# Kernel optimization log

Hardware: AMD Instinct MI355X
Metric: run time of the kernel (lower is better)

Reference implementation:

```python
import jax, jax.numpy as jnp
import numpy as np

B, S, D, H = 4, 2048, 1024, 16
DH = D // H  # attention_head_size = 64


def setup_inputs() -> dict:
    key = jax.random.key(0)
    ks = jax.random.split(key, 9)
    scale = 1.0 / np.sqrt(D)
    x = jax.random.normal(ks[0], (B, S, D), dtype=jnp.float32)
    Wq = jax.random.normal(ks[1], (H, D, DH), dtype=jnp.float32) * scale
    Wk = jax.random.normal(ks[2], (H, D, DH), dtype=jnp.float32) * scale
    Wv = jax.random.normal(ks[3], (H, D, DH), dtype=jnp.float32) * scale
    bq = jax.random.normal(ks[4], (H, DH), dtype=jnp.float32) * 0.01
    bk = jax.random.normal(ks[5], (H, DH), dtype=jnp.float32) * 0.01
    bv = jax.random.normal(ks[6], (H, DH), dtype=jnp.float32) * 0.01
    Wo = jax.random.normal(ks[7], (D, D), dtype=jnp.float32) * scale
    bo = jax.random.normal(ks[8], (D,), dtype=jnp.float32) * 0.01
    return {"x": x, "Wq": Wq, "bq": bq, "Wk": Wk, "bk": bk,
            "Wv": Wv, "bv": bv, "Wo": Wo, "bo": bo}


def reference(x, Wq, bq, Wk, bk, Wv, bv, Wo, bo):
    # Per-head Linear projections, stacked over the head axis h.
    q = jnp.einsum('bsd,hde->bhse', x, Wq) + bq[None, :, None, :]
    k = jnp.einsum('bsd,hde->bhse', x, Wk) + bk[None, :, None, :]
    v = jnp.einsum('bsd,hde->bhse', x, Wv) + bv[None, :, None, :]
    # QK^T / sqrt(dh), softmax over keys (axis=-1), then @ V.
    scores = jnp.einsum('bhse,bhte->bhst', q, k) / jnp.sqrt(jnp.float32(DH))
    attn = jax.nn.softmax(scores, axis=-1)
    ctx = jnp.einsum('bhst,bhte->bhse', attn, v)
    # Concatenate heads along the feature axis: [B,S,H*DH].
    concat = jnp.transpose(ctx, (0, 2, 1, 3)).reshape(B, S, H * DH)
    # Output projection (dropout is identity in inference).
    return concat @ Wo + bo
```

## Files before the change

### kernel.cpp

```cpp
#include <hip/hip_runtime.h>


#define Bn  4
#define Sn  2048
#define Dn  1024
#define Hn  16
#define DHn 64
#define Mn  (Bn*Sn)
#define LDKV 72

typedef unsigned short u16;
typedef __attribute__((ext_vector_type(8))) short short8;
typedef __attribute__((ext_vector_type(4))) short short4v;
typedef __attribute__((ext_vector_type(4))) float f32x4;
typedef __attribute__((ext_vector_type(2))) unsigned int uint2v;

__device__ __forceinline__ u16 f2bf(float f) {
  unsigned u = __float_as_uint(f);
  return (u16)((u + 0x7FFFu + ((u >> 16) & 1u)) >> 16);
}

__device__ __forceinline__ void async16(const void* g, void* l) {
  __builtin_amdgcn_global_load_lds(
      (const __attribute__((address_space(1))) void*)g,
      (__attribute__((address_space(3))) void*)l, 16, 0, 0);
}

__device__ __forceinline__ unsigned pk2(float a, float b) {
  return __builtin_amdgcn_perm(__float_as_uint(b), __float_as_uint(a), 0x07060302u);
}

__global__ __launch_bounds__(256) void k_convert_x(
    const float4* __restrict__ x, ushort4* __restrict__ xb, int n4) {
  int i = blockIdx.x * 256 + threadIdx.x;
  if (i < n4) {
    float4 f = x[i];
    ushort4 o;
    o.x = f2bf(f.x); o.y = f2bf(f.y); o.z = f2bf(f.z); o.w = f2bf(f.w);
    xb[i] = o;
  }
}

__global__ __launch_bounds__(256) void k_convert_w(
    const float* __restrict__ Wq, const float* __restrict__ Wk,
    const float* __restrict__ Wv, const float* __restrict__ Wo,
    u16* __restrict__ WqT, u16* __restrict__ WkT,
    u16* __restrict__ WvT, u16* __restrict__ WoT) {
  __shared__ float t[64][65];
  const int bid = blockIdx.x;
  const int wsel = bid >> 8;
  const int idx = bid & 255;
  const int tid = threadIdx.x;
  const int c = tid & 63;
  const int r4 = tid >> 6;

  if (wsel < 3) {
    const float* W = (wsel == 0) ? Wq : (wsel == 1) ? Wk : Wv;
    u16* T = (wsel == 0) ? WqT : (wsel == 1) ? WkT : WvT;
    const int h = idx >> 4;
    const int d0 = (idx & 15) * 64;
    const float* src = W + (size_t)h * (Dn * DHn) + (size_t)d0 * DHn;
#pragma unroll
    for (int r = 0; r < 16; r++) {
      int row = r * 4 + r4;
      t[row][c] = src[row * DHn + c];
    }
    __syncthreads();
    u16* dst = T + (size_t)(h * 64) * Dn + d0;
#pragma unroll
    for (int r = 0; r < 16; r++) {
      int erow = r * 4 + r4;
      dst[(size_t)erow * Dn + c] = f2bf(t[c][erow]);
    }
  } else {
    const int n0 = (idx >> 4) * 64;
    const int d0 = (idx & 15) * 64;
#pragma unroll
    for (int r = 0; r < 16; r++) {
      int row = r * 4 + r4;
      t[row][c] = Wo[(size_t)(d0 + row) * Dn + n0 + c];
    }
    __syncthreads();
#pragma unroll
    for (int r = 0; r < 16; r++) {
      int nrow = r * 4 + r4;
      WoT[(size_t)(n0 + nrow) * Dn + d0 + c] = f2bf(t[c][nrow]);
    }
  }
}

template<int SWAP>
__global__ __launch_bounds__(512) void k_gemm_qkv(
    const u16* __restrict__ A, const u16* __restrict__ B0T,
    const u16* __restrict__ B1T, const float* __restrict__ bias0,
    const float* __restrict__ bias1, u16* __restrict__ out0,
    u16* __restrict__ out1) {
  const int z = blockIdx.z;
  const u16* BT = z ? B1T : B0T;
  const float* bias = z ? bias1 : bias0;
  u16* dst = z ? out1 : out0;
  const int tile_m = blockIdx.x * 128;
  const int tile_n = blockIdx.y * 128;
  const int K = Dn;

  __shared__ u16 As[128 * 64];
  __shared__ u16 Bs[128 * 64];

  const int tid = threadIdx.x;
  const int lane = tid & 63;
  const int wave = tid >> 6;
  const int wm = wave & 3, wn = wave >> 2;
  const int quad = lane >> 4, l16 = lane & 15;
  const int srow8 = lane >> 3;
  const int gchunk = (lane & 7) ^ srow8;
  const int sw = l16 & 7;

  f32x4 acc[2][4];
#pragma unroll
  for (int i = 0; i < 2; i++)
#pragma unroll
    for (int j = 0; j < 4; j++) acc[i][j] = (f32x4){0.f, 0.f, 0.f, 0.f};

  for (int k0 = 0; k0 < K; k0 += 64) {
    const int rb = wave * 16;
    async16(&A[(size_t)(tile_m + rb + srow8) * K + k0 + gchunk * 8], &As[rb * 64]);
    async16(&A[(size_t)(tile_m + rb + 8 + srow8) * K + k0 + gchunk * 8], &As[(rb + 8) * 64]);
    async16(&BT[(size_t)(tile_n + rb + srow8) * K + k0 + gchunk * 8], &Bs[rb * 64]);
    async16(&BT[(size_t)(tile_n + rb + 8 + srow8) * K + k0 + gchunk * 8], &Bs[(rb + 8) * 64]);
    __syncthreads();
#pragma unroll
    for (int ks = 0; ks < 2; ++ks) {
      short8 a[2], b[4];
#pragma unroll
      for (int i = 0; i < 2; i++)
        a[i] = *(const short8*)&As[(wm * 32 + i * 16 + l16) * 64 + ((ks * 4 + quad) ^ sw) * 8];
#pragma unroll
      for (int j = 0; j < 4; j++)
        b[j] = *(const short8*)&Bs[(wn * 64 + j * 16 + l16) * 64 + ((ks * 4 + quad) ^ sw) * 8];
#pragma unroll
      for (int i = 0; i < 2; i++)
#pragma unroll
        for (int j = 0; j < 4; j++)
          acc[i][j] = SWAP
              ? __builtin_amdgcn_mfma_f32_16x16x32_bf16(b[j], a[i], acc[i][j], 0, 0, 0)
              : __builtin_amdgcn_mfma_f32_16x16x32_bf16(a[i], b[j], acc[i][j], 0, 0, 0);
    }
    __syncthreads();
  }

  if (SWAP) {
    const float scale = (z == 0) ? 0.18033688011112042f : 1.0f;
#pragma unroll
    for (int i = 0; i < 2; i++) {
      const int s = tile_m + wm * 32 + i * 16 + l16;
      const int bb = s >> 11, sl = s & 2047;
#pragma unroll
      for (int j = 0; j < 4; j++) {
        const int nb = tile_n + wn * 64 + j * 16 + quad * 4;
        const float4 b4 = *(const float4*)&bias[nb];
        const int h = nb >> 6, e0 = nb & 63;
        ushort4 o;
        o.x = f2bf((acc[i][j][0] + b4.x) * scale);
        o.y = f2bf((acc[i][j][1] + b4.y) * scale);
        o.z = f2bf((acc[i][j][2] + b4.z) * scale);
        o.w = f2bf((acc[i][j][3] + b4.w) * scale);
        *(ushort4*)&dst[((size_t)(bb * Hn + h) * Sn + sl) * DHn + e0] = o;
      }
    }
  } else {
#pragma unroll
    for (int i = 0; i < 2; i++) {
      const int s0 = tile_m + wm * 32 + i * 16 + quad * 4;
      const int bb = s0 >> 11, sl = s0 & 2047;
#pragma unroll
      for (int j = 0; j < 4; j++) {
        const int n = tile_n + wn * 64 + j * 16 + l16;
        const int h = n >> 6, e = n & 63;
        const float bn = bias[n];
        ushort4 o;
        o.x = f2bf(acc[i][j][0] + bn);
        o.y = f2bf(acc[i][j][1] + bn);
        o.z = f2bf(acc[i][j][2] + bn);
        o.w = f2bf(acc[i][j][3] + bn);
        *(ushort4*)&dst[((size_t)(bb * Hn + h) * DHn + e) * Sn + sl] = o;
      }
    }
  }
}

__global__ __launch_bounds__(256) void k_attn(
    const u16* __restrict__ qg, const u16* __restrict__ kg,
    const u16* __restrict__ vg, u16* __restrict__ ctx) {
  const int bh = blockIdx.y;
  const int b = bh >> 4, h = bh & 15;
  const int tid = threadIdx.x;
  const int wave = tid >> 6, lane = tid & 63;
  const int quad = lane >> 4, l16 = lane & 15;
  const int qbase = blockIdx.x * 128 + wave * 32;

  const u16* qp = qg + (size_t)bh * Sn * DHn;
  const u16* kp = kg + (size_t)bh * Sn * DHn;
  const u16* vp = vg + (size_t)bh * DHn * Sn;

  __shared__ u16 Ks[2][64 * 64];
  __shared__ u16 Vs[2][64 * LDKV];

  const int srow8 = lane >> 3;
  const int gchunk = (lane & 7) ^ srow8;
  const int sw = l16 & 7;

  const int vrow = tid >> 3;
  const int vc = tid & 7;

  short8 bq[2][2];
#pragma unroll
  for (int g2 = 0; g2 < 2; g2++) {
    bq[g2][0] = *(const short8*)&qp[(size_t)(qbase + g2 * 16 + l16) * DHn + quad * 8];
    bq[g2][1] = *(const short8*)&qp[(size_t)(qbase + g2 * 16 + l16) * DHn + 32 + quad * 8];
  }

  f32x4 octx[2][4];
#pragma unroll
  for (int g2 = 0; g2 < 2; g2++)
#pragma unroll
    for (int j = 0; j < 4; j++) octx[g2][j] = (f32x4){0.f, 0.f, 0.f, 0.f};
  float lr[2] = {0.f, 0.f};

  {
    const int rbase = wave * 16;
    async16(&kp[(size_t)(rbase + srow8) * DHn + gchunk * 8], &Ks[0][rbase * 64]);
    async16(&kp[(size_t)(rbase + 8 + srow8) * DHn + gchunk * 8], &Ks[0][(rbase + 8) * 64]);
    uint4 vv0 = *(const uint4*)&vp[(size_t)vrow * Sn + vc * 8];
    uint4 vv1 = *(const uint4*)&vp[(size_t)(32 + vrow) * Sn + vc * 8];
    *(uint4*)&Vs[0][vrow * LDKV + vc * 8] = vv0;
    *(uint4*)&Vs[0][(32 + vrow) * LDKV + vc * 8] = vv1;
  }
  __syncthreads();

  uint4 vv0, vv1;
  for (int kt = 0; kt < Sn / 64; ++kt) {
    const int cur = kt & 1, nxt = cur ^ 1;
    const bool more = (kt + 1 < Sn / 64);
    if (more) {
      const int key1 = (kt + 1) * 64;
      const int rbase = wave * 16;
      async16(&kp[(size_t)(key1 + rbase + srow8) * DHn + gchunk * 8], &Ks[nxt][rbase * 64]);
      async16(&kp[(size_t)(key1 + rbase + 8 + srow8) * DHn + gchunk * 8], &Ks[nxt][(rbase + 8) * 64]);
      vv0 = *(const uint4*)&vp[(size_t)vrow * Sn + key1 + vc * 8];
      vv1 = *(const uint4*)&vp[(size_t)(32 + vrow) * Sn + key1 + vc * 8];
    }

    short4v ap[2][4];
#pragma unroll
    for (int g = 0; g < 4; g++) {
      short8 ka0 = *(const short8*)&Ks[cur][(g * 16 + l16) * 64 + (quad ^ sw) * 8];
      short8 ka1 = *(const short8*)&Ks[cur][(g * 16 + l16) * 64 + ((quad + 4) ^ sw) * 8];
#pragma unroll
      for (int g2 = 0; g2 < 2; g2++) {
        f32x4 sc = (f32x4){0.f, 0.f, 0.f, 0.f};
        sc = __builtin_amdgcn_mfma_f32_16x16x32_bf16(ka0, bq[g2][0], sc, 0, 0, 0);
        sc = __builtin_amdgcn_mfma_f32_16x16x32_bf16(ka1, bq[g2][1], sc, 0, 0, 0);
        float p[4];
#pragma unroll
        for (int r = 0; r < 4; r++) p[r] = __builtin_amdgcn_exp2f(sc[r]);
        lr[g2] += (p[0] + p[1]) + (p[2] + p[3]);
        ap[g2][g] = __builtin_bit_cast(short4v,
            (uint2v){pk2(p[0], p[1]), pk2(p[2], p[3])});
      }
    }

#pragma unroll
    for (int j = 0; j < 4; j++) {
#pragma unroll
      for (int g = 0; g < 4; g++) {
        short4v vb = *(const short4v*)&Vs[cur][(j * 16 + l16) * LDKV + g * 16 + quad * 4];
        octx[0][j] = __builtin_amdgcn_mfma_f32_16x16x16bf16_1k(ap[0][g], vb, octx[0][j], 0, 0, 0);
        octx[1][j] = __builtin_amdgcn_mfma_f32_16x16x16bf16_1k(ap[1][g], vb, octx[1][j], 0, 0, 0);
      }
    }

    if (more) {
      *(uint4*)&Vs[nxt][vrow * LDKV + vc * 8] = vv0;
      *(uint4*)&Vs[nxt][(32 + vrow) * LDKV + vc * 8] = vv1;
    }
    __syncthreads();
  }

#pragma unroll
  for (int g2 = 0; g2 < 2; g2++) {
    lr[g2] += __shfl_xor(lr[g2], 16, 64);
    lr[g2] += __shfl_xor(lr[g2], 32, 64);
  }
  float rl[2][4];
#pragma unroll
  for (int g2 = 0; g2 < 2; g2++)
#pragma unroll
    for (int r = 0; r < 4; r++)
      rl[g2][r] = 1.0f / __shfl(lr[g2], quad * 4 + r, 64);

#pragma unroll
  for (int g2 = 0; g2 < 2; g2++)
#pragma unroll
    for (int j = 0; j < 4; j++) {
      const int n = h * DHn + j * 16 + l16;
#pragma unroll
      for (int r = 0; r < 4; r++) {
        const int s = qbase + g2 * 16 + quad * 4 + r;
        ctx[(size_t)(b * Sn + s) * Dn + n] = f2bf(octx[g2][j][r] * rl[g2][r]);
      }
    }
}

__global__ __launch_bounds__(512) void k_gemm_out(
    const u16* __restrict__ A, const u16* __restrict__ WoT,
    const float* __restrict__ bo, float* __restrict__ out) {
  const int tile_m = blockIdx.x * 128;
  const int tile_n = blockIdx.y * 128;
  const int K = Dn;

  __shared__ u16 As[128 * 64];
  __shared__ u16 Bs[128 * 64];

  const int tid = threadIdx.x;
  const int lane = tid & 63;
  const int wave = tid >> 6;
  const int wm = wave & 3, wn = wave >> 2;
  const int quad = lane >> 4, l16 = lane & 15;
  const int srow8 = lane >> 3;
  const int gchunk = (lane & 7) ^ srow8;
  const int sw = l16 & 7;

  f32x4 acc[2][4];
#pragma unroll
  for (int i = 0; i < 2; i++)
#pragma unroll
    for (int j = 0; j < 4; j++) acc[i][j] = (f32x4){0.f, 0.f, 0.f, 0.f};

  for (int k0 = 0; k0 < K; k0 += 64) {
    const int rb = wave * 16;
    async16(&A[(size_t)(tile_m + rb + srow8) * K + k0 + gchunk * 8], &As[rb * 64]);
    async16(&A[(size_t)(tile_m + rb + 8 + srow8) * K + k0 + gchunk * 8], &As[(rb + 8) * 64]);
    async16(&WoT[(size_t)(tile_n + rb + srow8) * K + k0 + gchunk * 8], &Bs[rb * 64]);
    async16(&WoT[(size_t)(tile_n + rb + 8 + srow8) * K + k0 + gchunk * 8], &Bs[(rb + 8) * 64]);
    __syncthreads();
#pragma unroll
    for (int ks = 0; ks < 2; ++ks) {
      short8 a[2], b[4];
#pragma unroll
      for (int i = 0; i < 2; i++)
        a[i] = *(const short8*)&As[(wm * 32 + i * 16 + l16) * 64 + ((ks * 4 + quad) ^ sw) * 8];
#pragma unroll
      for (int j = 0; j < 4; j++)
        b[j] = *(const short8*)&Bs[(wn * 64 + j * 16 + l16) * 64 + ((ks * 4 + quad) ^ sw) * 8];
#pragma unroll
      for (int i = 0; i < 2; i++)
#pragma unroll
        for (int j = 0; j < 4; j++)
          acc[i][j] = __builtin_amdgcn_mfma_f32_16x16x32_bf16(b[j], a[i], acc[i][j], 0, 0, 0);
    }
    __syncthreads();
  }

#pragma unroll
  for (int i = 0; i < 2; i++) {
    const int s = tile_m + wm * 32 + i * 16 + l16;
#pragma unroll
    for (int j = 0; j < 4; j++) {
      const int nb = tile_n + wn * 64 + j * 16 + quad * 4;
      const float4 b4 = *(const float4*)&bo[nb];
      float4 o;
      o.x = acc[i][j][0] + b4.x;
      o.y = acc[i][j][1] + b4.y;
      o.z = acc[i][j][2] + b4.z;
      o.w = acc[i][j][3] + b4.w;
      *(float4*)&out[(size_t)s * Dn + nb] = o;
    }
  }
}

extern "C" void kernel_launch(void* const* d_in, const int* in_sizes, int n_in,
                              void* d_out, int out_size, void* d_ws, size_t ws_size,
                              hipStream_t stream) {
  const float* x  = (const float*)d_in[0];
  const float* Wq = (const float*)d_in[1];
  const float* bq = (const float*)d_in[2];
  const float* Wk = (const float*)d_in[3];
  const float* bk = (const float*)d_in[4];
  const float* Wv = (const float*)d_in[5];
  const float* bv = (const float*)d_in[6];
  const float* Wo = (const float*)d_in[7];
  const float* bo = (const float*)d_in[8];
  float* out = (float*)d_out;

  char* ws = (char*)d_ws;
  u16* xb  = (u16*)ws;  ws += (size_t)Mn * Dn * 2;
  u16* WqT = (u16*)ws;  ws += (size_t)Dn * Dn * 2;
  u16* WkT = (u16*)ws;  ws += (size_t)Dn * Dn * 2;
  u16* WvT = (u16*)ws;  ws += (size_t)Dn * Dn * 2;
  u16* WoT = (u16*)ws;  ws += (size_t)Dn * Dn * 2;
  u16* qb  = (u16*)ws;  ws += (size_t)Mn * Dn * 2;
  u16* kb  = (u16*)ws;  ws += (size_t)Mn * Dn * 2;
  u16* vtb = (u16*)ws;  ws += (size_t)Mn * Dn * 2;
  u16* ctx = xb;

  k_convert_x<<<(Mn * Dn / 4) / 256, 256, 0, stream>>>((const float4*)x, (ushort4*)xb, Mn * Dn / 4);
  k_convert_w<<<1024, 256, 0, stream>>>(Wq, Wk, Wv, Wo, WqT, WkT, WvT, WoT);

  dim3 g1(Mn / 128, Dn / 128, 2);
  k_gemm_qkv<1><<<g1, 512, 0, stream>>>(xb, WqT, WkT, bq, bk, qb, kb);
  dim3 g1v(Mn / 128, Dn / 128, 1);
  k_gemm_qkv<0><<<g1v, 512, 0, stream>>>(xb, WvT, nullptr, bv, nullptr, vtb, nullptr);

  dim3 g2(Sn / 128, Bn * Hn);
  k_attn<<<g2, 256, 0, stream>>>(qb, kb, vtb, ctx);

  dim3 g3(Mn / 128, Dn / 128);
  k_gemm_out<<<g3, 512, 0, stream>>>(ctx, WoT, bo, out);
}
```

Measured before the change: 285.9 us.

## Split attention key tiles across two wave groups and load V asynchronously

The attention kernel now runs 512 threads per block. Two groups of four waves each take half of every 64-key tile, and their partial context and row sums are combined through shared memory at the end. V tiles are now loaded with async global-to-LDS copies into an XOR-swizzled layout, replacing the register-staged padded copy, and MFMA sections are wrapped in s_setprio. The aim is more waves in flight to hide latency and less register and VGPR traffic for V. The cost is an extra cross-group reduction and more synchronisation per block.

```diff
diff --git a/kernel.cpp b/kernel.cpp
--- a/kernel.cpp
+++ b/kernel.cpp
@@ -7,7 +7,6 @@
 #define Hn  16
 #define DHn 64
 #define Mn  (Bn*Sn)
-#define LDKV 72
 
 typedef unsigned short u16;
 typedef __attribute__((ext_vector_type(8))) short short8;
@@ -188,7 +187,7 @@
   }
 }
 
-__global__ __launch_bounds__(256) void k_attn(
+__global__ __launch_bounds__(512, 8) void k_attn(
     const u16* __restrict__ qg, const u16* __restrict__ kg,
     const u16* __restrict__ vg, u16* __restrict__ ctx) {
   const int bh = blockIdx.y;
@@ -196,21 +195,20 @@
   const int tid = threadIdx.x;
   const int wave = tid >> 6, lane = tid & 63;
   const int quad = lane >> 4, l16 = lane & 15;
-  const int qbase = blockIdx.x * 128 + wave * 32;
+  const int kh = wave >> 2;
+  const int qw = wave & 3;
+  const int qbase = blockIdx.x * 128 + qw * 32;
 
   const u16* qp = qg + (size_t)bh * Sn * DHn;
   const u16* kp = kg + (size_t)bh * Sn * DHn;
   const u16* vp = vg + (size_t)bh * DHn * Sn;
 
-  __shared__ u16 Ks[2][64 * 64];
-  __shared__ u16 Vs[2][64 * LDKV];
+  __shared__ u16 SM[4][64 * 64];
 
   const int srow8 = lane >> 3;
   const int gchunk = (lane & 7) ^ srow8;
   const int sw = l16 & 7;
-
-  const int vrow = tid >> 3;
-  const int vc = tid & 7;
+  const int rbase = wave * 8;
 
   short8 bq[2][2];
 #pragma unroll
@@ -226,40 +224,31 @@
     for (int j = 0; j < 4; j++) octx[g2][j] = (f32x4){0.f, 0.f, 0.f, 0.f};
   float lr[2] = {0.f, 0.f};
 
-  {
-    const int rbase = wave * 16;
-    async16(&kp[(size_t)(rbase + srow8) * DHn + gchunk * 8], &Ks[0][rbase * 64]);
-    async16(&kp[(size_t)(rbase + 8 + srow8) * DHn + gchunk * 8], &Ks[0][(rbase + 8) * 64]);
-    uint4 vv0 = *(const uint4*)&vp[(size_t)vrow * Sn + vc * 8];
-    uint4 vv1 = *(const uint4*)&vp[(size_t)(32 + vrow) * Sn + vc * 8];
-    *(uint4*)&Vs[0][vrow * LDKV + vc * 8] = vv0;
-    *(uint4*)&Vs[0][(32 + vrow) * LDKV + vc * 8] = vv1;
-  }
+  async16(&kp[(size_t)(rbase + srow8) * DHn + gchunk * 8], &SM[0][rbase * 64]);
+  async16(&vp[(size_t)(rbase + srow8) * Sn + gchunk * 8], &SM[2][rbase * 64]);
   __syncthreads();
 
-  uint4 vv0, vv1;
   for (int kt = 0; kt < Sn / 64; ++kt) {
     const int cur = kt & 1, nxt = cur ^ 1;
-    const bool more = (kt + 1 < Sn / 64);
-    if (more) {
+    if (kt + 1 < Sn / 64) {
       const int key1 = (kt + 1) * 64;
-      const int rbase = wave * 16;
-      async16(&kp[(size_t)(key1 + rbase + srow8) * DHn + gchunk * 8], &Ks[nxt][rbase * 64]);
-      async16(&kp[(size_t)(key1 + rbase + 8 + srow8) * DHn + gchunk * 8], &Ks[nxt][(rbase + 8) * 64]);
-      vv0 = *(const uint4*)&vp[(size_t)vrow * Sn + key1 + vc * 8];
-      vv1 = *(const uint4*)&vp[(size_t)(32 + vrow) * Sn + key1 + vc * 8];
-    }
-
-    short4v ap[2][4];
-#pragma unroll
-    for (int g = 0; g < 4; g++) {
-      short8 ka0 = *(const short8*)&Ks[cur][(g * 16 + l16) * 64 + (quad ^ sw) * 8];
-      short8 ka1 = *(const short8*)&Ks[cur][(g * 16 + l16) * 64 + ((quad + 4) ^ sw) * 8];
+      async16(&kp[(size_t)(key1 + rbase + srow8) * DHn + gchunk * 8], &SM[nxt][rbase * 64]);
+      async16(&vp[(size_t)(rbase + srow8) * Sn + key1 + gchunk * 8], &SM[2 + nxt][rbase * 64]);
+    }
+
+    short4v ap[2][2];
+#pragma unroll
+    for (int g = 0; g < 2; g++) {
+      const int krow = kh * 32 + g * 16 + l16;
+      short8 ka0 = *(const short8*)&SM[cur][krow * 64 + (quad ^ sw) * 8];
+      short8 ka1 = *(const short8*)&SM[cur][krow * 64 + ((quad + 4) ^ sw) * 8];
 #pragma unroll
       for (int g2 = 0; g2 < 2; g2++) {
         f32x4 sc = (f32x4){0.f, 0.f, 0.f, 0.f};
+        __builtin_amdgcn_s_setprio(1);
         sc = __builtin_amdgcn_mfma_f32_16x16x32_bf16(ka0, bq[g2][0], sc, 0, 0, 0);
         sc = __builtin_amdgcn_mfma_f32_16x16x32_bf16(ka1, bq[g2][1], sc, 0, 0, 0);
+        __builtin_amdgcn_s_setprio(0);
         float p[4];
 #pragma unroll
         for (int r = 0; r < 4; r++) p[r] = __builtin_amdgcn_exp2f(sc[r]);
@@ -269,22 +258,44 @@
       }
     }
 
+    __builtin_amdgcn_s_setprio(1);
 #pragma unroll
     for (int j = 0; j < 4; j++) {
 #pragma unroll
-      for (int g = 0; g < 4; g++) {
-        short4v vb = *(const short4v*)&Vs[cur][(j * 16 + l16) * LDKV + g * 16 + quad * 4];
+      for (int g = 0; g < 2; g++) {
+        short4v vb = *(const short4v*)&SM[2 + cur][(j * 16 + l16) * 64 +
+            (((kh * 4 + g * 2 + (quad >> 1)) ^ sw) * 8) + (quad & 1) * 4];
         octx[0][j] = __builtin_amdgcn_mfma_f32_16x16x16bf16_1k(ap[0][g], vb, octx[0][j], 0, 0, 0);
         octx[1][j] = __builtin_amdgcn_mfma_f32_16x16x16bf16_1k(ap[1][g], vb, octx[1][j], 0, 0, 0);
       }
     }
-
-    if (more) {
-      *(uint4*)&Vs[nxt][vrow * LDKV + vc * 8] = vv0;
-      *(uint4*)&Vs[nxt][(32 + vrow) * LDKV + vc * 8] = vv1;
-    }
-    __syncthreads();
-  }
+    __builtin_amdgcn_s_setprio(0);
+    __syncthreads();
+  }
+
+  float* mbuf = (float*)&SM[0][0];
+  float* lrbuf = mbuf + 4096;
+#pragma unroll
+  for (int g2 = 0; g2 < 2; g2++) {
+    __syncthreads();
+    if (kh == 1) {
+#pragma unroll
+      for (int j = 0; j < 4; j++)
+        *(f32x4*)&mbuf[((qw * 4 + j) * 64 + lane) * 4] = octx[g2][j];
+      lrbuf[qw * 64 + lane] = lr[g2];
+    }
+    __syncthreads();
+    if (kh == 0) {
+#pragma unroll
+      for (int j = 0; j < 4; j++) {
+        f32x4 o = *(const f32x4*)&mbuf[((qw * 4 + j) * 64 + lane) * 4];
+        octx[g2][j][0] += o[0]; octx[g2][j][1] += o[1];
+        octx[g2][j][2] += o[2]; octx[g2][j][3] += o[3];
+      }
+      lr[g2] += lrbuf[qw * 64 + lane];
+    }
+  }
+  if (kh) return;
 
 #pragma unroll
   for (int g2 = 0; g2 < 2; g2++) {
@@ -412,7 +423,7 @@
   k_gemm_qkv<0><<<g1v, 512, 0, stream>>>(xb, WvT, nullptr, bv, nullptr, vtb, nullptr);
 
   dim3 g2(Sn / 128, Bn * Hn);
-  k_attn<<<g2, 256, 0, stream>>>(qb, kb, vtb, ctx);
+  k_attn<<<g2, 512, 0, stream>>>(qb, kb, vtb, ctx);
 
   dim3 g3(Mn / 128, Dn / 128);
   k_gemm_out<<<g3, 512, 0, stream>>>(ctx, WoT, bo, out);
```

New measurement: 841.2 us. 194% more time.

## Halve attention query tile per block and single-buffer V in shared memory

Applied to the files above, without the earlier changes.

Each attention wave now handles 16 query rows instead of 32, so a block covers 64 queries and the grid doubles along the sequence axis. V goes from a double-buffered LDS tile to a single buffer, with an extra barrier before the next V tile is written. This raises block count and occupancy and cuts registers and LDS per block. In exchange, K/V tiles are loaded from global memory twice as often per query, and each iteration adds a synchronization.

```diff
diff --git a/kernel.cpp b/kernel.cpp
--- a/kernel.cpp
+++ b/kernel.cpp
@@ -196,14 +196,14 @@
   const int tid = threadIdx.x;
   const int wave = tid >> 6, lane = tid & 63;
   const int quad = lane >> 4, l16 = lane & 15;
-  const int qbase = blockIdx.x * 128 + wave * 32;
+  const int qbase = blockIdx.x * 64 + wave * 16;
 
   const u16* qp = qg + (size_t)bh * Sn * DHn;
   const u16* kp = kg + (size_t)bh * Sn * DHn;
   const u16* vp = vg + (size_t)bh * DHn * Sn;
 
   __shared__ u16 Ks[2][64 * 64];
-  __shared__ u16 Vs[2][64 * LDKV];
+  __shared__ u16 Vs[64 * LDKV];
 
   const int srow8 = lane >> 3;
   const int gchunk = (lane & 7) ^ srow8;
@@ -212,28 +212,22 @@
   const int vrow = tid >> 3;
   const int vc = tid & 7;
 
-  short8 bq[2][2];
-#pragma unroll
-  for (int g2 = 0; g2 < 2; g2++) {
-    bq[g2][0] = *(const short8*)&qp[(size_t)(qbase + g2 * 16 + l16) * DHn + quad * 8];
-    bq[g2][1] = *(const short8*)&qp[(size_t)(qbase + g2 * 16 + l16) * DHn + 32 + quad * 8];
-  }
-
-  f32x4 octx[2][4];
-#pragma unroll
-  for (int g2 = 0; g2 < 2; g2++)
-#pragma unroll
-    for (int j = 0; j < 4; j++) octx[g2][j] = (f32x4){0.f, 0.f, 0.f, 0.f};
-  float lr[2] = {0.f, 0.f};
+  short8 bq0 = *(const short8*)&qp[(size_t)(qbase + l16) * DHn + quad * 8];
+  short8 bq1 = *(const short8*)&qp[(size_t)(qbase + l16) * DHn + 32 + quad * 8];
+
+  f32x4 octx[4];
+#pragma unroll
+  for (int j = 0; j < 4; j++) octx[j] = (f32x4){0.f, 0.f, 0.f, 0.f};
+  float lr = 0.f;
 
   {
     const int rbase = wave * 16;
     async16(&kp[(size_t)(rbase + srow8) * DHn + gchunk * 8], &Ks[0][rbase * 64]);
     async16(&kp[(size_t)(rbase + 8 + srow8) * DHn + gchunk * 8], &Ks[0][(rbase + 8) * 64]);
-    uint4 vv0 = *(const uint4*)&vp[(size_t)vrow * Sn + vc * 8];
-    uint4 vv1 = *(const uint4*)&vp[(size_t)(32 + vrow) * Sn + vc * 8];
-    *(uint4*)&Vs[0][vrow * LDKV + vc * 8] = vv0;
-    *(uint4*)&Vs[0][(32 + vrow) * LDKV + vc * 8] = vv1;
+    uint4 v0 = *(const uint4*)&vp[(size_t)vrow * Sn + vc * 8];
+    uint4 v1 = *(const uint4*)&vp[(size_t)(32 + vrow) * Sn + vc * 8];
+    *(uint4*)&Vs[vrow * LDKV + vc * 8] = v0;
+    *(uint4*)&Vs[(32 + vrow) * LDKV + vc * 8] = v1;
   }
   __syncthreads();
 
@@ -250,65 +244,54 @@
       vv1 = *(const uint4*)&vp[(size_t)(32 + vrow) * Sn + key1 + vc * 8];
     }
 
-    short4v ap[2][4];
+    short4v ap[4];
 #pragma unroll
     for (int g = 0; g < 4; g++) {
       short8 ka0 = *(const short8*)&Ks[cur][(g * 16 + l16) * 64 + (quad ^ sw) * 8];
       short8 ka1 = *(const short8*)&Ks[cur][(g * 16 + l16) * 64 + ((quad + 4) ^ sw) * 8];
-#pragma unroll
-      for (int g2 = 0; g2 < 2; g2++) {
-        f32x4 sc = (f32x4){0.f, 0.f, 0.f, 0.f};
-        sc = __builtin_amdgcn_mfma_f32_16x16x32_bf16(ka0, bq[g2][0], sc, 0, 0, 0);
-        sc = __builtin_amdgcn_mfma_f32_16x16x32_bf16(ka1, bq[g2][1], sc, 0, 0, 0);
-        float p[4];
-#pragma unroll
-        for (int r = 0; r < 4; r++) p[r] = __builtin_amdgcn_exp2f(sc[r]);
-        lr[g2] += (p[0] + p[1]) + (p[2] + p[3]);
-        ap[g2][g] = __builtin_bit_cast(short4v,
-            (uint2v){pk2(p[0], p[1]), pk2(p[2], p[3])});
+      f32x4 sc = (f32x4){0.f, 0.f, 0.f, 0.f};
+      sc = __builtin_amdgcn_mfma_f32_16x16x32_bf16(ka0, bq0, sc, 0, 0, 0);
+      sc = __builtin_amdgcn_mfma_f32_16x16x32_bf16(ka1, bq1, sc, 0, 0, 0);
+      float p[4];
+#pragma unroll
+      for (int r = 0; r < 4; r++) p[r] = __builtin_amdgcn_exp2f(sc[r]);
+      lr += (p[0] + p[1]) + (p[2] + p[3]);
+      ap[g] = __builtin_bit_cast(short4v, (uint2v){pk2(p[0], p[1]), pk2(p[2], p[3])});
+    }
+
+#pragma unroll
+    for (int j = 0; j < 4; j++) {
+#pragma unroll
+      for (int g = 0; g < 4; g++) {
+        short4v vb = *(const short4v*)&Vs[(j * 16 + l16) * LDKV + g * 16 + quad * 4];
+        octx[j] = __builtin_amdgcn_mfma_f32_16x16x16bf16_1k(ap[g], vb, octx[j], 0, 0, 0);
       }
     }
 
-#pragma unroll
-    for (int j = 0; j < 4; j++) {
-#pragma unroll
-      for (int g = 0; g < 4; g++) {
-        short4v vb = *(const short4v*)&Vs[cur][(j * 16 + l16) * LDKV + g * 16 + quad * 4];
-        octx[0][j] = __builtin_amdgcn_mfma_f32_16x16x16bf16_1k(ap[0][g], vb, octx[0][j], 0, 0, 0);
-        octx[1][j] = __builtin_amdgcn_mfma_f32_16x16x16bf16_1k(ap[1][g], vb, octx[1][j], 0, 0, 0);
-      }
-    }
-
+    __syncthreads();
     if (more) {
-      *(uint4*)&Vs[nxt][vrow * LDKV + vc * 8] = vv0;
-      *(uint4*)&Vs[nxt][(32 + vrow) * LDKV + vc * 8] = vv1;
-    }
-    __syncthreads();
-  }
-
-#pragma unroll
-  for (int g2 = 0; g2 < 2; g2++) {
-    lr[g2] += __shfl_xor(lr[g2], 16, 64);
-    lr[g2] += __shfl_xor(lr[g2], 32, 64);
-  }
-  float rl[2][4];
-#pragma unroll
-  for (int g2 = 0; g2 < 2; g2++)
-#pragma unroll
-    for (int r = 0; r < 4; r++)
-      rl[g2][r] = 1.0f / __shfl(lr[g2], quad * 4 + r, 64);
-
-#pragma unroll
-  for (int g2 = 0; g2 < 2; g2++)
-#pragma unroll
-    for (int j = 0; j < 4; j++) {
-      const int n = h * DHn + j * 16 + l16;
-#pragma unroll
-      for (int r = 0; r < 4; r++) {
-        const int s = qbase + g2 * 16 + quad * 4 + r;
-        ctx[(size_t)(b * Sn + s) * Dn + n] = f2bf(octx[g2][j][r] * rl[g2][r]);
-      }
-    }
+      *(uint4*)&Vs[vrow * LDKV + vc * 8] = vv0;
+      *(uint4*)&Vs[(32 + vrow) * LDKV + vc * 8] = vv1;
+    }
+    __syncthreads();
+  }
+
+  lr += __shfl_xor(lr, 16, 64);
+  lr += __shfl_xor(lr, 32, 64);
+  float rl[4];
+#pragma unroll
+  for (int r = 0; r < 4; r++)
+    rl[r] = 1.0f / __shfl(lr, quad * 4 + r, 64);
+
+#pragma unroll
+  for (int j = 0; j < 4; j++) {
+    const int n = h * DHn + j * 16 + l16;
+#pragma unroll
+    for (int r = 0; r < 4; r++) {
+      const int s = qbase + quad * 4 + r;
+      ctx[(size_t)(b * Sn + s) * Dn + n] = f2bf(octx[j][r] * rl[r]);
+    }
+  }
 }
 
 __global__ __launch_bounds__(512) void k_gemm_out(
@@ -411,7 +394,7 @@
   dim3 g1v(Mn / 128, Dn / 128, 1);
   k_gemm_qkv<0><<<g1v, 512, 0, stream>>>(xb, WvT, nullptr, bv, nullptr, vtb, nullptr);
 
-  dim3 g2(Sn / 128, Bn * Hn);
+  dim3 g2(Sn / 64, Bn * Hn);
   k_attn<<<g2, 256, 0, stream>>>(qb, kb, vtb, ctx);
 
   dim3 g3(Mn / 128, Dn / 128);
```

After: 308.6 us. 1.08x slower.

## Split key tiles across wave pairs in attention kernel and merge partial results

Applied to the files above, without the earlier changes.

The attention kernel now gives each block 64 queries instead of 128 and splits every 64-key tile between two wave pairs, each handling 32 keys. The partial context accumulators and row sums are merged through shared memory at the end, and the grid doubles. V storage drops to a single buffer, which needs an extra barrier per iteration. The goal is more blocks and more parallelism per head, at the cost of reloading K/V tiles twice as often per query and extra synchronisation.

```diff
diff --git a/kernel.cpp b/kernel.cpp
--- a/kernel.cpp
+++ b/kernel.cpp
@@ -196,14 +196,16 @@
   const int tid = threadIdx.x;
   const int wave = tid >> 6, lane = tid & 63;
   const int quad = lane >> 4, l16 = lane & 15;
-  const int qbase = blockIdx.x * 128 + wave * 32;
+  const int kh = wave >> 1;
+  const int qw = wave & 1;
+  const int qbase = blockIdx.x * 64 + qw * 32;
 
   const u16* qp = qg + (size_t)bh * Sn * DHn;
   const u16* kp = kg + (size_t)bh * Sn * DHn;
   const u16* vp = vg + (size_t)bh * DHn * Sn;
 
   __shared__ u16 Ks[2][64 * 64];
-  __shared__ u16 Vs[2][64 * LDKV];
+  __shared__ u16 Vs[64 * LDKV];
 
   const int srow8 = lane >> 3;
   const int gchunk = (lane & 7) ^ srow8;
@@ -230,10 +232,10 @@
     const int rbase = wave * 16;
     async16(&kp[(size_t)(rbase + srow8) * DHn + gchunk * 8], &Ks[0][rbase * 64]);
     async16(&kp[(size_t)(rbase + 8 + srow8) * DHn + gchunk * 8], &Ks[0][(rbase + 8) * 64]);
-    uint4 vv0 = *(const uint4*)&vp[(size_t)vrow * Sn + vc * 8];
-    uint4 vv1 = *(const uint4*)&vp[(size_t)(32 + vrow) * Sn + vc * 8];
-    *(uint4*)&Vs[0][vrow * LDKV + vc * 8] = vv0;
-    *(uint4*)&Vs[0][(32 + vrow) * LDKV + vc * 8] = vv1;
+    uint4 v0 = *(const uint4*)&vp[(size_t)vrow * Sn + vc * 8];
+    uint4 v1 = *(const uint4*)&vp[(size_t)(32 + vrow) * Sn + vc * 8];
+    *(uint4*)&Vs[vrow * LDKV + vc * 8] = v0;
+    *(uint4*)&Vs[(32 + vrow) * LDKV + vc * 8] = v1;
   }
   __syncthreads();
 
@@ -250,11 +252,12 @@
       vv1 = *(const uint4*)&vp[(size_t)(32 + vrow) * Sn + key1 + vc * 8];
     }
 
-    short4v ap[2][4];
-#pragma unroll
-    for (int g = 0; g < 4; g++) {
-      short8 ka0 = *(const short8*)&Ks[cur][(g * 16 + l16) * 64 + (quad ^ sw) * 8];
-      short8 ka1 = *(const short8*)&Ks[cur][(g * 16 + l16) * 64 + ((quad + 4) ^ sw) * 8];
+    short4v ap[2][2];
+#pragma unroll
+    for (int g = 0; g < 2; g++) {
+      const int krow = kh * 32 + g * 16 + l16;
+      short8 ka0 = *(const short8*)&Ks[cur][krow * 64 + (quad ^ sw) * 8];
+      short8 ka1 = *(const short8*)&Ks[cur][krow * 64 + ((quad + 4) ^ sw) * 8];
 #pragma unroll
       for (int g2 = 0; g2 < 2; g2++) {
         f32x4 sc = (f32x4){0.f, 0.f, 0.f, 0.f};
@@ -264,26 +267,51 @@
 #pragma unroll
         for (int r = 0; r < 4; r++) p[r] = __builtin_amdgcn_exp2f(sc[r]);
         lr[g2] += (p[0] + p[1]) + (p[2] + p[3]);
-        ap[g2][g] = __builtin_bit_cast(short4v,
-            (uint2v){pk2(p[0], p[1]), pk2(p[2], p[3])});
+        ap[g2][g] = __builtin_bit_cast(short4v, (uint2v){pk2(p[0], p[1]), pk2(p[2], p[3])});
       }
     }
 
 #pragma unroll
     for (int j = 0; j < 4; j++) {
 #pragma unroll
-      for (int g = 0; g < 4; g++) {
-        short4v vb = *(const short4v*)&Vs[cur][(j * 16 + l16) * LDKV + g * 16 + quad * 4];
+      for (int g = 0; g < 2; g++) {
+        short4v vb = *(const short4v*)&Vs[(j * 16 + l16) * LDKV + kh * 32 + g * 16 + quad * 4];
         octx[0][j] = __builtin_amdgcn_mfma_f32_16x16x16bf16_1k(ap[0][g], vb, octx[0][j], 0, 0, 0);
         octx[1][j] = __builtin_amdgcn_mfma_f32_16x16x16bf16_1k(ap[1][g], vb, octx[1][j], 0, 0, 0);
       }
     }
 
+    __syncthreads();
     if (more) {
-      *(uint4*)&Vs[nxt][vrow * LDKV + vc * 8] = vv0;
-      *(uint4*)&Vs[nxt][(32 + vrow) * LDKV + vc * 8] = vv1;
-    }
-    __syncthreads();
+      *(uint4*)&Vs[vrow * LDKV + vc * 8] = vv0;
+      *(uint4*)&Vs[(32 + vrow) * LDKV + vc * 8] = vv1;
+    }
+    __syncthreads();
+  }
+
+  float* mbuf = (float*)&Ks[0][0];
+  float* lrbuf = (float*)&Vs[0];
+  if (kh == 1) {
+#pragma unroll
+    for (int g2 = 0; g2 < 2; g2++) {
+#pragma unroll
+      for (int j = 0; j < 4; j++)
+        *(f32x4*)&mbuf[(((qw * 2 + g2) * 4 + j) * 64 + lane) * 4] = octx[g2][j];
+      lrbuf[(qw * 2 + g2) * 64 + lane] = lr[g2];
+    }
+  }
+  __syncthreads();
+  if (kh == 1) return;
+
+#pragma unroll
+  for (int g2 = 0; g2 < 2; g2++) {
+#pragma unroll
+    for (int j = 0; j < 4; j++) {
+      f32x4 o = *(const f32x4*)&mbuf[(((qw * 2 + g2) * 4 + j) * 64 + lane) * 4];
+      octx[g2][j][0] += o[0]; octx[g2][j][1] += o[1];
+      octx[g2][j][2] += o[2]; octx[g2][j][3] += o[3];
+    }
+    lr[g2] += lrbuf[(qw * 2 + g2) * 64 + lane];
   }
 
 #pragma unroll
@@ -411,7 +439,7 @@
   dim3 g1v(Mn / 128, Dn / 128, 1);
   k_gemm_qkv<0><<<g1v, 512, 0, stream>>>(xb, WvT, nullptr, bv, nullptr, vtb, nullptr);
 
-  dim3 g2(Sn / 128, Bn * Hn);
+  dim3 g2(Sn / 64, Bn * Hn);
   k_attn<<<g2, 256, 0, stream>>>(qb, kb, vtb, ctx);
 
   dim3 g3(Mn / 128, Dn / 128);
```

Result: slower. 307.3 us (+7.5%).
